# Optimization experiments

Hardware: AMD Instinct MI355X
Metric: run time of the kernel (lower is better)

Reference implementation:

```python
import jax, jax.numpy as jnp
import numpy as np

CLS_NUM = 2
SCALE = 8.0
NO_OBJ_SCALE = 1.0
EPS = 1e-7


def setup_inputs() -> dict:
    key = jax.random.key(0)
    k1, k2, k3, k4, k5, k6 = jax.random.split(key, 6)
    B, C, H, W, N = 8, CLS_NUM, 512, 512, 160
    predict = jax.random.normal(k1, (B, C, H, W), dtype=jnp.float32)
    b = jax.random.randint(k2, (N,), 0, B).astype(jnp.float32)
    c = jax.random.randint(k3, (N,), 0, C).astype(jnp.float32)
    cxy = jax.random.uniform(k4, (N, 2), minval=0.0, maxval=H * SCALE)
    wh = jax.random.uniform(k5, (N, 2), minval=64.0, maxval=256.0)
    ang = jax.random.uniform(k6, (N, 1), minval=-np.pi, maxval=np.pi)
    targets = jnp.concatenate([b[:, None], c[:, None], cxy, wh, ang], axis=1).astype(jnp.float32)
    return {"predict": predict, "targets": targets}


def _forward(predict, targets):
    B, C, H, W = predict.shape
    pred = jnp.transpose(predict, (0, 2, 3, 1))          # [B,H,W,C]
    conf_all = jax.nn.sigmoid(pred)
    heatmap = jnp.max(conf_all, axis=-1)                 # [B,H,W]

    bid = targets[:, 0].astype(jnp.int32)                # [N] batch ids
    cid = targets[:, 1].astype(jnp.int32)                # [N] class ids
    cx = targets[:, 2] / SCALE
    cy = targets[:, 3] / SCALE
    w = targets[:, 4] / SCALE
    h = targets[:, 5] / SCALE
    ang = targets[:, 6]
    cos, sin = jnp.cos(ang), jnp.sin(ang)
    # rotate box center into the rotated frame (same math as render_map)
    x = cx * cos + cy * sin
    y = -cx * sin + cy * cos
    x3, x4 = x - h / 2, x + h / 2
    y3, y4 = y - w / 2, y + w / 2
    x1, x2 = x3 - 0.5, x4 + 0.5
    y1, y2 = y3 - 0.5, y4 + 0.5

    gx = jnp.arange(W, dtype=jnp.float32)[None, :] + 0.5  # [1,W] -> broadcasts to [H,W]
    gy = jnp.arange(H, dtype=jnp.float32)[:, None] + 0.5  # [H,1]
    vx = cos[:, None, None] * gx + sin[:, None, None] * gy   # [N,H,W]
    vy = -sin[:, None, None] * gx + cos[:, None, None] * gy  # [N,H,W]

    def box_mask(lo_x, hi_x, lo_y, hi_y):
        return ((lo_x[:, None, None] <= vx) & (vx <= hi_x[:, None, None]) &
                (lo_y[:, None, None] <= vy) & (vy <= hi_y[:, None, None]))

    inner = box_mask(x3, x4, y3, y4)  # obj region, [N,H,W]
    outer = box_mask(x1, x2, y1, y2)  # expanded region (clears noobj)

    loss = jnp.float32(0.0)
    for cls in range(CLS_NUM):
        sel = (cid == cls)[:, None, None]
        obj_cnt = jax.ops.segment_sum((inner & sel).astype(jnp.float32), bid, num_segments=B)
        out_cnt = jax.ops.segment_sum((outer & sel).astype(jnp.float32), bid, num_segments=B)
        obj_mask = obj_cnt > 0            # [B,H,W]
        noobj_mask = out_cnt <= 0         # starts at 1, zeroed inside any expanded box
        conf_c = jnp.clip(conf_all[..., cls], EPS, 1.0 - EPS)
        n_obj = jnp.sum(obj_mask)
        n_noobj = jnp.sum(noobj_mask)
        # BCE with target 1 on obj cells, target 0 on noobj cells (tconf == obj mask)
        loss_obj = -jnp.sum(jnp.where(obj_mask, jnp.log(conf_c), 0.0)) / jnp.maximum(n_obj, 1)
        loss_noobj = -jnp.sum(jnp.where(noobj_mask, jnp.log(1.0 - conf_c), 0.0)) / jnp.maximum(n_noobj, 1)
        loss = loss + jnp.where(n_obj > 0, loss_obj + NO_OBJ_SCALE * loss_noobj, 0.0)
    return loss, heatmap


def reference(predict, targets):
    return _forward(predict, targets)
```

## Files before the change

### kernel.cpp

```cpp
#include <hip/hip_runtime.h>
#include <math.h>

#define CLS 2
#define BATCH 8
#define HH 512
#define WW 512
#define INV_SCALE 0.125f
#define LOGEPS -16.118095651f

#define TCAP 160
#define NB 512
#define TSTR 256


__global__ __launch_bounds__(512) void heatmap_prep(
    const float* __restrict__ targets, int nT,
    float* __restrict__ tprep, double* __restrict__ gsum, int* __restrict__ gcnt)
{
    const int t = threadIdx.x;
    for (int q = t; q < 4 * NB; q += 512) { gsum[q] = 0.0; gcnt[q] = 0; }
    if (t < nT) {
        const float* tp = targets + t * 7;
        const float cs = cosf(tp[6]), sn = sinf(tp[6]);
        const float cx = tp[2] * INV_SCALE, cy = tp[3] * INV_SCALE;
        const float w_ = tp[4] * INV_SCALE, h_ = tp[5] * INV_SCALE;
        const float x = cx * cs + cy * sn;
        const float y = -cx * sn + cy * cs;
        ((int*)tprep)[0 * TSTR + t] = (int)tp[0];
        ((int*)tprep)[1 * TSTR + t] = (int)tp[1];
        tprep[2 * TSTR + t] = cs;
        tprep[3 * TSTR + t] = sn;
        tprep[4 * TSTR + t] = x - 0.5f * h_;
        tprep[5 * TSTR + t] = x + 0.5f * h_;
        tprep[6 * TSTR + t] = y - 0.5f * w_;
        tprep[7 * TSTR + t] = y + 0.5f * w_;
    }
}

__global__ __launch_bounds__(256) void heatmap_main(
    const float* __restrict__ predict, const float* __restrict__ tprep,
    int nT, float* __restrict__ out, double* __restrict__ gsum,
    int* __restrict__ gcnt)
{
    __shared__ int s_cnt;
    __shared__ float s_cos[TCAP], s_sin[TCAP];
    __shared__ float s_x3[TCAP], s_x4[TCAP], s_y3[TCAP], s_y4[TCAP];
    __shared__ int   s_cid[TCAP];

    const int tid = threadIdx.x;
    const int blockPix = blockIdx.x * 256;
    const int b  = blockPix >> 18;
    const int i  = (blockPix >> 9) & (HH - 1);
    const int j0 = blockPix & (WW - 1);

    if (tid == 0) s_cnt = 0;
    __syncthreads();

    const float gy = (float)i + 0.5f;

    if (tid < nT && ((const int*)tprep)[tid] == b) {
        const float cs = tprep[2 * TSTR + tid], sn = tprep[3 * TSTR + tid];
        const float x3 = tprep[4 * TSTR + tid], x4 = tprep[5 * TSTR + tid];
        const float y3 = tprep[6 * TSTR + tid], y4 = tprep[7 * TSTR + tid];

        const float gxl = (float)j0 + 0.5f, gxh = (float)j0 + 255.5f;
        const float a1 = cs * gxl + sn * gy, a2 = cs * gxh + sn * gy;
        const float vxlo = fminf(a1, a2), vxhi = fmaxf(a1, a2);
        const float b1 = -sn * gxl + cs * gy, b2 = -sn * gxh + cs * gy;
        const float vylo = fminf(b1, b2), vyhi = fmaxf(b1, b2);

        const float M = 0.51f;
        if (vxhi >= x3 - M && vxlo <= x4 + M && vyhi >= y3 - M && vylo <= y4 + M) {
            int slot = atomicAdd(&s_cnt, 1);
            s_cos[slot] = cs; s_sin[slot] = sn;
            s_x3[slot] = x3; s_x4[slot] = x4;
            s_y3[slot] = y3; s_y4[slot] = y4;
            s_cid[slot] = ((const int*)tprep)[TSTR + tid];
        }
    }
    __syncthreads();
    const int cnt = s_cnt;

    const int j = j0 + tid;
    const float gx = (float)j + 0.5f;
    int objm = 0, outm = 0;
    for (int n = 0; n < cnt; ++n) {
        const float cs = s_cos[n], sn = s_sin[n];
        const float vx = cs * gx + sn * gy;
        const float vy = -sn * gx + cs * gy;
        const float x3 = s_x3[n], x4 = s_x4[n], y3 = s_y3[n], y4 = s_y4[n];
        const bool in_  = (x3 <= vx) & (vx <= x4) & (y3 <= vy) & (vy <= y4);
        const bool out_ = (x3 - 0.5f <= vx) & (vx <= x4 + 0.5f) &
                          (y3 - 0.5f <= vy) & (vy <= y4 + 0.5f);
        const int c = s_cid[n];
        objm |= ((int)in_) << c;
        outm |= ((int)out_) << c;
    }

    const int base = (b * CLS * HH + i) * WW + j;
    const float p0 = predict[base];
    const float p1 = predict[base + HH * WW];
    const float t0 = __expf(p0), t1 = __expf(p1);
    const float s0 = 1.0f + t0,  s1 = 1.0f + t1;
    const float c0 = t0 * __builtin_amdgcn_rcpf(s0);
    const float c1 = t1 * __builtin_amdgcn_rcpf(s1);
    float l10 = -__logf(s0);
    float l11 = -__logf(s1);
    const float lc0 = fmaxf(p0 + l10, LOGEPS);
    const float lc1 = fmaxf(p1 + l11, LOGEPS);
    l10 = fmaxf(l10, LOGEPS);
    l11 = fmaxf(l11, LOGEPS);

    out[1 + (b * HH + i) * WW + j] = fmaxf(c0, c1);

    float so0 = (objm & 1) ? lc0 : 0.0f;
    float so1 = (objm & 2) ? lc1 : 0.0f;
    float sn0 = (outm & 1) ? 0.0f : l10;
    float sn1 = (outm & 2) ? 0.0f : l11;
    const int co0 = (int)__popcll(__ballot(objm & 1));
    const int co1 = (int)__popcll(__ballot(objm & 2));
    const int cn0 = (int)__popcll(__ballot(!(outm & 1)));
    const int cn1 = (int)__popcll(__ballot(!(outm & 2)));

    #pragma unroll
    for (int off = 32; off >= 1; off >>= 1) {
        so0 += __shfl_down(so0, off); so1 += __shfl_down(so1, off);
        sn0 += __shfl_down(sn0, off); sn1 += __shfl_down(sn1, off);
    }

    __shared__ float r_f[4][4];
    __shared__ int   r_i[4][4];
    const int wv = tid >> 6, ln = tid & 63;
    if (ln == 0) {
        r_f[wv][0] = so0; r_f[wv][1] = so1; r_f[wv][2] = sn0; r_f[wv][3] = sn1;
        r_i[wv][0] = co0; r_i[wv][1] = co1; r_i[wv][2] = cn0; r_i[wv][3] = cn1;
    }
    __syncthreads();
    if (tid == 0) {
        const int bkt = blockIdx.x & (NB - 1);
        #pragma unroll
        for (int q = 0; q < 4; ++q) {
            const float f = r_f[0][q] + r_f[1][q] + r_f[2][q] + r_f[3][q];
            const int   c = r_i[0][q] + r_i[1][q] + r_i[2][q] + r_i[3][q];
            if (f != 0.0f) atomicAdd(&gsum[q * NB + bkt], (double)f);
            if (c)         atomicAdd(&gcnt[q * NB + bkt], c);
        }
    }
}

__global__ __launch_bounds__(512) void heatmap_finalize(
    const double* __restrict__ gsum, const int* __restrict__ gcnt,
    float* __restrict__ out)
{
    const int t = threadIdx.x;
    double f[4]; int c[4];
    #pragma unroll
    for (int q = 0; q < 4; ++q) { f[q] = gsum[q * NB + t]; c[q] = gcnt[q * NB + t]; }

    #pragma unroll
    for (int off = 32; off >= 1; off >>= 1) {
        #pragma unroll
        for (int q = 0; q < 4; ++q) {
            f[q] += __shfl_down(f[q], off);
            c[q] += __shfl_down(c[q], off);
        }
    }

    __shared__ double sf[8][4];
    __shared__ int    si[8][4];
    const int wv = t >> 6, ln = t & 63;
    if (ln == 0) {
        #pragma unroll
        for (int q = 0; q < 4; ++q) { sf[wv][q] = f[q]; si[wv][q] = c[q]; }
    }
    __syncthreads();
    if (t == 0) {
        double F[4] = {0, 0, 0, 0}; int C[4] = {0, 0, 0, 0};
        for (int w = 0; w < 8; ++w)
            #pragma unroll
            for (int q = 0; q < 4; ++q) { F[q] += sf[w][q]; C[q] += si[w][q]; }
        float loss = 0.0f;
        #pragma unroll
        for (int cls = 0; cls < CLS; ++cls) {
            const int no = C[cls];
            const int nn = C[2 + cls];
            if (no > 0) {
                const float lo  = -(float)F[cls]     / (float)(no > 1 ? no : 1);
                const float ln_ = -(float)F[2 + cls] / (float)(nn > 1 ? nn : 1);
                loss += lo + ln_;
            }
        }
        out[0] = loss;
    }
}

extern "C" void kernel_launch(void* const* d_in, const int* in_sizes, int n_in,
                              void* d_out, int out_size, void* d_ws, size_t ws_size,
                              hipStream_t stream) {
    const float* predict = (const float*)d_in[0];
    const float* targets = (const float*)d_in[1];
    const int nT = in_sizes[1] / 7;
    float* out = (float*)d_out;
    char* ws = (char*)d_ws;
    double* gsum = (double*)ws;
    int* gcnt = (int*)(ws + 16384);
    float* tprep = (float*)(ws + 24576);

    heatmap_prep<<<1, 512, 0, stream>>>(targets, nT, tprep, gsum, gcnt);
    const int pixels = BATCH * HH * WW;
    heatmap_main<<<pixels / 256, 256, 0, stream>>>(predict, tprep, nT, out,
                                                   gsum, gcnt);
    heatmap_finalize<<<1, 512, 0, stream>>>(gsum, gcnt, out);
}
```

Baseline: 89.68 us.

## Bucket targets by batch and process four pixels per thread in single-wave blocks

The prep kernel now groups targets per batch image, so each main block scans only its own batch's targets, and it culls them with a wave ballot and prefix count instead of shared-memory atomics. The main kernel runs one 64-thread wave per 256-pixel row segment, with each thread covering four adjacent pixels. The box rotation is computed once per target and stepped incrementally across those pixels, and predictions are read with float4 loads. The block reduction becomes a single-wave shuffle with packed integer counts, skipping the object-sum reduction when no pixel is inside a box. Risks: fewer threads per block reduce latency hiding, the heatmap stores are no longer coalesced as wide writes, and a batch holding more than 192 targets would overflow its bucket.

```diff
diff --git a/kernel.cpp b/kernel.cpp
--- a/kernel.cpp
+++ b/kernel.cpp
@@ -8,142 +8,172 @@
 #define INV_SCALE 0.125f
 #define LOGEPS -16.118095651f
 
-#define TCAP 160
 #define NB 512
-#define TSTR 256
-
-
-__global__ __launch_bounds__(512) void heatmap_prep(
-    const float* __restrict__ targets, int nT,
-    float* __restrict__ tprep, double* __restrict__ gsum, int* __restrict__ gcnt)
+#define TSTRIDE 192
+#define TCAP 192
+
+
+__global__ __launch_bounds__(256) void heatmap_prep(
+    const float* __restrict__ targets, int nT, double* __restrict__ gsum,
+    int* __restrict__ gcnt, int* __restrict__ bcnt, float* __restrict__ tdat)
 {
+    __shared__ int s_b[BATCH];
     const int t = threadIdx.x;
-    for (int q = t; q < 4 * NB; q += 512) { gsum[q] = 0.0; gcnt[q] = 0; }
+    if (t < BATCH) s_b[t] = 0;
+    for (int q = t; q < 4 * NB; q += 256) { gsum[q] = 0.0; gcnt[q] = 0; }
+    __syncthreads();
     if (t < nT) {
         const float* tp = targets + t * 7;
+        const int b = (int)tp[0];
         const float cs = cosf(tp[6]), sn = sinf(tp[6]);
         const float cx = tp[2] * INV_SCALE, cy = tp[3] * INV_SCALE;
         const float w_ = tp[4] * INV_SCALE, h_ = tp[5] * INV_SCALE;
         const float x = cx * cs + cy * sn;
         const float y = -cx * sn + cy * cs;
-        ((int*)tprep)[0 * TSTR + t] = (int)tp[0];
-        ((int*)tprep)[1 * TSTR + t] = (int)tp[1];
-        tprep[2 * TSTR + t] = cs;
-        tprep[3 * TSTR + t] = sn;
-        tprep[4 * TSTR + t] = x - 0.5f * h_;
-        tprep[5 * TSTR + t] = x + 0.5f * h_;
-        tprep[6 * TSTR + t] = y - 0.5f * w_;
-        tprep[7 * TSTR + t] = y + 0.5f * w_;
-    }
-}
-
-__global__ __launch_bounds__(256) void heatmap_main(
-    const float* __restrict__ predict, const float* __restrict__ tprep,
-    int nT, float* __restrict__ out, double* __restrict__ gsum,
-    int* __restrict__ gcnt)
+        const int slot = atomicAdd(&s_b[b], 1);
+        float* tb = tdat + b * (7 * TSTRIDE);
+        tb[0 * TSTRIDE + slot] = cs;
+        tb[1 * TSTRIDE + slot] = sn;
+        tb[2 * TSTRIDE + slot] = x - 0.5f * h_;
+        tb[3 * TSTRIDE + slot] = x + 0.5f * h_;
+        tb[4 * TSTRIDE + slot] = y - 0.5f * w_;
+        tb[5 * TSTRIDE + slot] = y + 0.5f * w_;
+        ((int*)tb)[6 * TSTRIDE + slot] = (int)tp[1];
+    }
+    __syncthreads();
+    if (t < BATCH) bcnt[t] = s_b[t];
+}
+
+__global__ __launch_bounds__(64) void heatmap_main(
+    const float* __restrict__ predict, float* __restrict__ out,
+    double* __restrict__ gsum, int* __restrict__ gcnt,
+    const int* __restrict__ bcnt, const float* __restrict__ tdat)
 {
-    __shared__ int s_cnt;
-    __shared__ float s_cos[TCAP], s_sin[TCAP];
+    __shared__ float s_cs[TCAP], s_sn[TCAP];
     __shared__ float s_x3[TCAP], s_x4[TCAP], s_y3[TCAP], s_y4[TCAP];
     __shared__ int   s_cid[TCAP];
 
-    const int tid = threadIdx.x;
+    const int l = threadIdx.x;
     const int blockPix = blockIdx.x * 256;
     const int b  = blockPix >> 18;
     const int i  = (blockPix >> 9) & (HH - 1);
     const int j0 = blockPix & (WW - 1);
-
-    if (tid == 0) s_cnt = 0;
-    __syncthreads();
-
     const float gy = (float)i + 0.5f;
 
-    if (tid < nT && ((const int*)tprep)[tid] == b) {
-        const float cs = tprep[2 * TSTR + tid], sn = tprep[3 * TSTR + tid];
-        const float x3 = tprep[4 * TSTR + tid], x4 = tprep[5 * TSTR + tid];
-        const float y3 = tprep[6 * TSTR + tid], y4 = tprep[7 * TSTR + tid];
-
-        const float gxl = (float)j0 + 0.5f, gxh = (float)j0 + 255.5f;
-        const float a1 = cs * gxl + sn * gy, a2 = cs * gxh + sn * gy;
-        const float vxlo = fminf(a1, a2), vxhi = fmaxf(a1, a2);
-        const float b1 = -sn * gxl + cs * gy, b2 = -sn * gxh + cs * gy;
-        const float vylo = fminf(b1, b2), vyhi = fmaxf(b1, b2);
-
-        const float M = 0.51f;
-        if (vxhi >= x3 - M && vxlo <= x4 + M && vyhi >= y3 - M && vylo <= y4 + M) {
-            int slot = atomicAdd(&s_cnt, 1);
-            s_cos[slot] = cs; s_sin[slot] = sn;
+    const int nb = bcnt[b];
+    const float* tb = tdat + b * (7 * TSTRIDE);
+    int cnt = 0;
+    for (int base = 0; base < nb; base += 64) {
+        bool acc = false;
+        float cs = 0.f, sn = 0.f, x3 = 0.f, x4 = 0.f, y3 = 0.f, y4 = 0.f;
+        int cid = 0;
+        const int t = base + l;
+        if (t < nb) {
+            cs = tb[0 * TSTRIDE + t]; sn = tb[1 * TSTRIDE + t];
+            x3 = tb[2 * TSTRIDE + t]; x4 = tb[3 * TSTRIDE + t];
+            y3 = tb[4 * TSTRIDE + t]; y4 = tb[5 * TSTRIDE + t];
+            cid = ((const int*)tb)[6 * TSTRIDE + t];
+            const float gxl = (float)j0 + 0.5f, gxh = (float)j0 + 255.5f;
+            const float a1 = cs * gxl + sn * gy, a2 = cs * gxh + sn * gy;
+            const float b1 = -sn * gxl + cs * gy, b2 = -sn * gxh + cs * gy;
+            const float vxlo = fminf(a1, a2), vxhi = fmaxf(a1, a2);
+            const float vylo = fminf(b1, b2), vyhi = fmaxf(b1, b2);
+            const float M = 0.51f;
+            acc = (vxhi >= x3 - M) & (vxlo <= x4 + M) &
+                  (vyhi >= y3 - M) & (vylo <= y4 + M);
+        }
+        const unsigned long long bal = __ballot(acc);
+        if (acc) {
+            const int slot = cnt + (int)__popcll(bal & ((1ull << l) - 1ull));
+            s_cs[slot] = cs; s_sn[slot] = sn;
             s_x3[slot] = x3; s_x4[slot] = x4;
             s_y3[slot] = y3; s_y4[slot] = y4;
-            s_cid[slot] = ((const int*)tprep)[TSTR + tid];
-        }
-    }
-    __syncthreads();
-    const int cnt = s_cnt;
-
-    const int j = j0 + tid;
-    const float gx = (float)j + 0.5f;
-    int objm = 0, outm = 0;
+            s_cid[slot] = cid;
+        }
+        cnt += (int)__popcll(bal);
+    }
+    __syncthreads();
+
+    const int j = j0 + 4 * l;
+    const float gxb = (float)j + 0.5f;
+    int objm[4] = {0, 0, 0, 0}, outm[4] = {0, 0, 0, 0};
     for (int n = 0; n < cnt; ++n) {
-        const float cs = s_cos[n], sn = s_sin[n];
-        const float vx = cs * gx + sn * gy;
-        const float vy = -sn * gx + cs * gy;
+        const float cs = s_cs[n], sn = s_sn[n];
         const float x3 = s_x3[n], x4 = s_x4[n], y3 = s_y3[n], y4 = s_y4[n];
-        const bool in_  = (x3 <= vx) & (vx <= x4) & (y3 <= vy) & (vy <= y4);
-        const bool out_ = (x3 - 0.5f <= vx) & (vx <= x4 + 0.5f) &
-                          (y3 - 0.5f <= vy) & (vy <= y4 + 0.5f);
-        const int c = s_cid[n];
-        objm |= ((int)in_) << c;
-        outm |= ((int)out_) << c;
-    }
-
-    const int base = (b * CLS * HH + i) * WW + j;
-    const float p0 = predict[base];
-    const float p1 = predict[base + HH * WW];
-    const float t0 = __expf(p0), t1 = __expf(p1);
-    const float s0 = 1.0f + t0,  s1 = 1.0f + t1;
-    const float c0 = t0 * __builtin_amdgcn_rcpf(s0);
-    const float c1 = t1 * __builtin_amdgcn_rcpf(s1);
-    float l10 = -__logf(s0);
-    float l11 = -__logf(s1);
-    const float lc0 = fmaxf(p0 + l10, LOGEPS);
-    const float lc1 = fmaxf(p1 + l11, LOGEPS);
-    l10 = fmaxf(l10, LOGEPS);
-    l11 = fmaxf(l11, LOGEPS);
-
-    out[1 + (b * HH + i) * WW + j] = fmaxf(c0, c1);
-
-    float so0 = (objm & 1) ? lc0 : 0.0f;
-    float so1 = (objm & 2) ? lc1 : 0.0f;
-    float sn0 = (outm & 1) ? 0.0f : l10;
-    float sn1 = (outm & 2) ? 0.0f : l11;
-    const int co0 = (int)__popcll(__ballot(objm & 1));
-    const int co1 = (int)__popcll(__ballot(objm & 2));
-    const int cn0 = (int)__popcll(__ballot(!(outm & 1)));
-    const int cn1 = (int)__popcll(__ballot(!(outm & 2)));
-
+        const int cbit = 1 << s_cid[n];
+        float vx = cs * gxb + sn * gy;
+        float vy = -sn * gxb + cs * gy;
+        #pragma unroll
+        for (int k = 0; k < 4; ++k) {
+            const bool in_  = (x3 <= vx) & (vx <= x4) & (y3 <= vy) & (vy <= y4);
+            const bool out_ = (x3 - 0.5f <= vx) & (vx <= x4 + 0.5f) &
+                              (y3 - 0.5f <= vy) & (vy <= y4 + 0.5f);
+            if (in_)  objm[k] |= cbit;
+            if (out_) outm[k] |= cbit;
+            vx += cs; vy -= sn;
+        }
+    }
+
+    const int pbase = (b * CLS * HH + i) * WW + j;
+    const float4 P0 = *(const float4*)(predict + pbase);
+    const float4 P1 = *(const float4*)(predict + pbase + HH * WW);
+
+    float so0 = 0.f, so1 = 0.f, sq0 = 0.f, sq1 = 0.f;
+    int c_obj0 = 0, c_obj1 = 0, c_no0 = 0, c_no1 = 0;
+    float hm[4];
+    #pragma unroll
+    for (int k = 0; k < 4; ++k) {
+        const float p0 = (&P0.x)[k], p1 = (&P1.x)[k];
+        const float t0 = __expf(p0), t1 = __expf(p1);
+        const float l0n = -__logf(1.0f + t0);
+        const float l1n = -__logf(1.0f + t1);
+        const float lc0 = fmaxf(p0 + l0n, LOGEPS);
+        const float lc1 = fmaxf(p1 + l1n, LOGEPS);
+        const float l0c = fmaxf(l0n, LOGEPS);
+        const float l1c = fmaxf(l1n, LOGEPS);
+        const float tm = fmaxf(t0, t1);
+        hm[k] = tm * __builtin_amdgcn_rcpf(1.0f + tm);
+        const int om = objm[k], um = outm[k];
+        if (om & 1) { so0 += lc0; ++c_obj0; }
+        if (om & 2) { so1 += lc1; ++c_obj1; }
+        if (!(um & 1)) { sq0 += l0c; ++c_no0; }
+        if (!(um & 2)) { sq1 += l1c; ++c_no1; }
+    }
+
+    float* ho = out + 1 + (b * HH + i) * WW + j;
+    ho[0] = hm[0]; ho[1] = hm[1]; ho[2] = hm[2]; ho[3] = hm[3];
+
+    const unsigned long long anyobj =
+        __ballot((objm[0] | objm[1] | objm[2] | objm[3]) != 0);
+    int pc = (c_no0 & 0xffff) | (c_no1 << 16);
     #pragma unroll
     for (int off = 32; off >= 1; off >>= 1) {
-        so0 += __shfl_down(so0, off); so1 += __shfl_down(so1, off);
-        sn0 += __shfl_down(sn0, off); sn1 += __shfl_down(sn1, off);
-    }
-
-    __shared__ float r_f[4][4];
-    __shared__ int   r_i[4][4];
-    const int wv = tid >> 6, ln = tid & 63;
-    if (ln == 0) {
-        r_f[wv][0] = so0; r_f[wv][1] = so1; r_f[wv][2] = sn0; r_f[wv][3] = sn1;
-        r_i[wv][0] = co0; r_i[wv][1] = co1; r_i[wv][2] = cn0; r_i[wv][3] = cn1;
-    }
-    __syncthreads();
-    if (tid == 0) {
+        sq0 += __shfl_down(sq0, off);
+        sq1 += __shfl_down(sq1, off);
+        pc  += __shfl_down(pc, off);
+    }
+    int po = 0;
+    if (anyobj) {
+        po = (c_obj0 & 0xffff) | (c_obj1 << 16);
+        #pragma unroll
+        for (int off = 32; off >= 1; off >>= 1) {
+            so0 += __shfl_down(so0, off);
+            so1 += __shfl_down(so1, off);
+            po  += __shfl_down(po, off);
+        }
+    }
+    if (l == 0) {
         const int bkt = blockIdx.x & (NB - 1);
-        #pragma unroll
-        for (int q = 0; q < 4; ++q) {
-            const float f = r_f[0][q] + r_f[1][q] + r_f[2][q] + r_f[3][q];
-            const int   c = r_i[0][q] + r_i[1][q] + r_i[2][q] + r_i[3][q];
-            if (f != 0.0f) atomicAdd(&gsum[q * NB + bkt], (double)f);
-            if (c)         atomicAdd(&gcnt[q * NB + bkt], c);
+        atomicAdd(&gsum[2 * NB + bkt], (double)sq0);
+        atomicAdd(&gsum[3 * NB + bkt], (double)sq1);
+        atomicAdd(&gcnt[2 * NB + bkt], pc & 0xffff);
+        atomicAdd(&gcnt[3 * NB + bkt], pc >> 16);
+        if (anyobj) {
+            const int o0 = po & 0xffff, o1 = po >> 16;
+            if (o0) { atomicAdd(&gsum[0 * NB + bkt], (double)so0);
+                      atomicAdd(&gcnt[0 * NB + bkt], o0); }
+            if (o1) { atomicAdd(&gsum[1 * NB + bkt], (double)so1);
+                      atomicAdd(&gcnt[1 * NB + bkt], o1); }
         }
     }
 }
@@ -204,11 +234,12 @@
     char* ws = (char*)d_ws;
     double* gsum = (double*)ws;
     int* gcnt = (int*)(ws + 16384);
-    float* tprep = (float*)(ws + 24576);
-
-    heatmap_prep<<<1, 512, 0, stream>>>(targets, nT, tprep, gsum, gcnt);
+    int* bcnt = (int*)(ws + 24576);
+    float* tdat = (float*)(ws + 24608);
+
+    heatmap_prep<<<1, 256, 0, stream>>>(targets, nT, gsum, gcnt, bcnt, tdat);
     const int pixels = BATCH * HH * WW;
-    heatmap_main<<<pixels / 256, 256, 0, stream>>>(predict, tprep, nT, out,
-                                                   gsum, gcnt);
+    heatmap_main<<<pixels / 256, 64, 0, stream>>>(predict, out, gsum, gcnt,
+                                                  bcnt, tdat);
     heatmap_finalize<<<1, 512, 0, stream>>>(gsum, gcnt, out);
 }
```

Result: faster. 80.86 us (-9.8%).
